# Optimization experiments

Hardware: AMD Instinct MI355X
Metric: run time of the kernel (lower is better)

## Reference

```python
import jax, jax.numpy as jnp
import numpy as np
from jax import lax

DIM, N_STATE, DT_RANK = 1024, 16, 64
BATCH, SEQ = 2, 2048


def setup_inputs() -> dict:
    key = jax.random.key(0)
    ks = jax.random.split(key, 12)
    s = 0.02
    x = jax.random.normal(ks[0], (BATCH, SEQ, DIM), dtype=jnp.float32)
    in_proj_w = jax.random.normal(ks[1], (2 * DIM, DIM), dtype=jnp.float32) * s
    conv_w = jax.random.normal(ks[2], (DIM, 1, 3), dtype=jnp.float32) * s
    conv_b = jax.random.normal(ks[3], (DIM,), dtype=jnp.float32) * s
    A_log = jax.random.normal(ks[4], (DIM, N_STATE), dtype=jnp.float32) * s
    D_param = jax.random.normal(ks[5], (DIM,), dtype=jnp.float32) * s
    x_proj_w = jax.random.normal(ks[6], (DT_RANK + 2 * N_STATE, DIM), dtype=jnp.float32) * s
    # dt_proj init mimics the torch module: bias = inv-softplus of dt in [dt_min, dt_max]
    dt = jnp.exp(jax.random.uniform(ks[7], (DIM,)) * (np.log(0.1) - np.log(0.001)) + np.log(0.001))
    dt = jnp.clip(dt, 0.0001, None)
    inv_dt = dt + jnp.log(-jnp.expm1(-dt))
    dt_init_std = DT_RANK ** (-0.5)
    dt_proj_w = jnp.tile(inv_dt[:, None], (1, DT_RANK)) * dt_init_std
    dt_proj_b = inv_dt
    out_proj_w = jax.random.normal(ks[8], (DIM, DIM), dtype=jnp.float32) * s
    return {
        "x": x, "in_proj_w": in_proj_w, "conv_w": conv_w, "conv_b": conv_b,
        "A_log": A_log, "D_param": D_param, "x_proj_w": x_proj_w,
        "dt_proj_w": dt_proj_w, "dt_proj_b": dt_proj_b, "out_proj_w": out_proj_w,
    }


def _selective_scan(u, delta, A, Bp, Cp, D_param):
    # u, delta: (B, L, D); A: (D, N); Bp, Cp: (B, L, N)
    deltaA = jnp.exp(delta[..., None] * A)                       # (B, L, D, N)
    deltaB_u = delta[..., None] * Bp[:, :, None, :] * u[..., None]  # (B, L, D, N)

    def step(state, inputs):
        dA_t, dBu_t, C_t = inputs          # (B, D, N), (B, D, N), (B, N)
        state = dA_t * state + dBu_t       # (B, D, N)
        y_t = jnp.einsum("bdn,bn->bd", state, C_t)
        return state, y_t

    init = jnp.zeros((u.shape[0], u.shape[2], A.shape[1]), dtype=u.dtype)
    xs = (jnp.swapaxes(deltaA, 0, 1), jnp.swapaxes(deltaB_u, 0, 1), jnp.swapaxes(Cp, 0, 1))
    _, ys = lax.scan(step, init, xs)       # ys: (L, B, D)
    y = jnp.swapaxes(ys, 0, 1)             # (B, L, D)
    return y + u * D_param


def reference(x, in_proj_w, conv_w, conv_b, A_log, D_param, x_proj_w, dt_proj_w, dt_proj_b, out_proj_w):
    B, L, D = x.shape
    xz = x @ in_proj_w.T                   # (B, L, 2D)
    xc, z = jnp.split(xz, 2, axis=-1)
    # depthwise conv1d, kernel 3, padding 1 (output length == L)
    xc = jnp.swapaxes(xc, 1, 2)            # (B, D, L)
    xc = lax.conv_general_dilated(
        xc, conv_w, window_strides=(1,), padding=[(1, 1)],
        dimension_numbers=("NCH", "OIH", "NCH"), feature_group_count=D,
    ) + conv_b[None, :, None]
    xc = jnp.swapaxes(xc, 1, 2)            # (B, L, D)
    x_dbl = xc @ x_proj_w.T                # (B, L, dt_rank + 2N)
    dt_r, Bp, Cp = jnp.split(x_dbl, [DT_RANK, DT_RANK + N_STATE], axis=-1)
    delta = jax.nn.softplus(dt_r @ dt_proj_w.T + dt_proj_b)   # (B, L, D)
    A = -jnp.exp(A_log)                    # (D, N)
    y = _selective_scan(xc, delta, A, Bp, Cp, D_param)
    y = y * jax.nn.silu(z)
    return y @ out_proj_w.T
```

## Files before the change

kernel.cpp:

```cpp
#include <hip/hip_runtime.h>
#include <math.h>

#define BATCH 2
#define SEQ   2048
#define DIM   1024
#define NST   16
#define DTR   64
#define KSL   8

typedef _Float16 f16x8 __attribute__((ext_vector_type(8)));
typedef float f32x4 __attribute__((ext_vector_type(4)));

__device__ __forceinline__ float softplus_f(float v) {
  return fmaxf(v, 0.f) + log1pf(expf(-fabsf(v)));
}
__device__ __forceinline__ float silu_f(float v) {
  return v / (1.f + expf(-v));
}

__device__ __forceinline__ void gl_lds16(const _Float16* g, _Float16* l) {
  __builtin_amdgcn_global_load_lds(
      (const __attribute__((address_space(1))) void*)g,
      (__attribute__((address_space(3))) void*)l, 16, 0, 0);
}

#define FMA_ROW(i, av)                                        \
  acc[i][0] = fmaf(av, b.x, acc[i][0]);                       \
  acc[i][1] = fmaf(av, b.y, acc[i][1]);                       \
  acc[i][2] = fmaf(av, b.z, acc[i][2]);                       \
  acc[i][3] = fmaf(av, b.w, acc[i][3]);

__global__ __launch_bounds__(256) void k_cvt(const float* __restrict__ in,
                                             _Float16* __restrict__ hi,
                                             _Float16* __restrict__ lo,
                                             int n) {
  const int i = (blockIdx.x * 256 + threadIdx.x) * 8;
  if (i >= n) return;
  const float4 a = *(const float4*)(in + i);
  const float4 b = *(const float4*)(in + i + 4);
  const float v[8] = {a.x, a.y, a.z, a.w, b.x, b.y, b.z, b.w};
  f16x8 h, l;
#pragma unroll
  for (int j = 0; j < 8; ++j) {
    const _Float16 hh = (_Float16)v[j];
    h[j] = hh;
    l[j] = (_Float16)(v[j] - (float)hh);
  }
  *(f16x8*)(hi + i) = h;
  *(f16x8*)(lo + i) = l;
}

template <int EPI>
__global__ __launch_bounds__(256) void kgemm_f16x3(
    const _Float16* __restrict__ Ah, const _Float16* __restrict__ Al,
    const _Float16* __restrict__ Bh, const _Float16* __restrict__ Bl,
    float* __restrict__ out0, float* __restrict__ out1) {
  __shared__ _Float16 sm[16384];
  _Float16* Ash = sm;
  _Float16* Asl = sm + 4096;
  _Float16* Bsh = sm + 8192;
  _Float16* Bsl = sm + 12288;

  const int tid = threadIdx.x;
  const int wid = tid >> 6, lane = tid & 63;
  const int wm = wid >> 1, wn = wid & 1;
  const int m0 = blockIdx.y * 128;
  const int n0 = blockIdx.x * 128;

  const int r0 = wid * 32;
  const int srow = lane >> 2;
  const int skq = (lane & 3) * 8;
  const _Float16* gAh = Ah + (size_t)(m0 + r0 + srow) * 1024 + skq;
  const _Float16* gAl = Al + (size_t)(m0 + r0 + srow) * 1024 + skq;
  const _Float16* gBh = Bh + (size_t)(n0 + r0 + srow) * 1024 + skq;
  const _Float16* gBl = Bl + (size_t)(n0 + r0 + srow) * 1024 + skq;
  _Float16* lAh = Ash + r0 * 32;
  _Float16* lAl = Asl + r0 * 32;
  _Float16* lBh = Bsh + r0 * 32;
  _Float16* lBl = Bsl + r0 * 32;

  const int fr = lane & 15;
  const int fk = (lane >> 4) * 8;

  f32x4 acc[4][4];
#pragma unroll
  for (int i = 0; i < 4; ++i)
#pragma unroll
    for (int j = 0; j < 4; ++j) acc[i][j] = (f32x4)(0.f);

  for (int k0 = 0; k0 < 1024; k0 += 32) {
    __syncthreads();
    gl_lds16(gAh + k0, lAh);
    gl_lds16(gAh + k0 + 16 * 1024, lAh + 512);
    gl_lds16(gAl + k0, lAl);
    gl_lds16(gAl + k0 + 16 * 1024, lAl + 512);
    gl_lds16(gBh + k0, lBh);
    gl_lds16(gBh + k0 + 16 * 1024, lBh + 512);
    gl_lds16(gBl + k0, lBl);
    gl_lds16(gBl + k0 + 16 * 1024, lBl + 512);
    __syncthreads();

    f16x8 ah[4], alo[4], bh[4], blo[4];
#pragma unroll
    for (int i = 0; i < 4; ++i) {
      const int ao = (wm * 64 + i * 16 + fr) * 32 + fk;
      const int bo = (wn * 64 + i * 16 + fr) * 32 + fk;
      ah[i]  = *(const f16x8*)(Ash + ao);
      alo[i] = *(const f16x8*)(Asl + ao);
      bh[i]  = *(const f16x8*)(Bsh + bo);
      blo[i] = *(const f16x8*)(Bsl + bo);
    }
#pragma unroll
    for (int i = 0; i < 4; ++i)
#pragma unroll
      for (int j = 0; j < 4; ++j) {
        acc[i][j] = __builtin_amdgcn_mfma_f32_16x16x32_f16(ah[i], bh[j],
                                                           acc[i][j], 0, 0, 0);
        acc[i][j] = __builtin_amdgcn_mfma_f32_16x16x32_f16(ah[i], blo[j],
                                                           acc[i][j], 0, 0, 0);
        acc[i][j] = __builtin_amdgcn_mfma_f32_16x16x32_f16(alo[i], bh[j],
                                                           acc[i][j], 0, 0, 0);
      }
  }

  const int lr4 = (lane >> 4) * 4, lc = lane & 15;
#pragma unroll
  for (int i = 0; i < 4; ++i) {
#pragma unroll
    for (int j = 0; j < 4; ++j) {
      const int ar = m0 + wm * 64 + i * 16 + lr4;
      const int bc = n0 + wn * 64 + j * 16 + lc;
#pragma unroll
      for (int r = 0; r < 4; ++r) {
        const float v = acc[i][j][r];
        if (EPI == 0) {
          out0[(size_t)(ar + r) * 1024 + bc] = v;
        } else {
          const int bb = bc >> 11, tt = bc & 2047;
          if (ar < 1024) {
            out0[((size_t)bb * 1024 + ar + r) * 2048 + tt] = v;
          } else {
            out1[((size_t)bb * 1024 + (ar + r - 1024)) * 2048 + tt] = v;
          }
        }
      }
    }
  }
}

__global__ __launch_bounds__(256) void k_conv(
    const float* __restrict__ xcraw, const float* __restrict__ cw,
    const float* __restrict__ cb, float* __restrict__ xc) {
  const int idx = blockIdx.x * 256 + threadIdx.x;
  const int t0 = (idx & (SEQ / 4 - 1)) * 4;
  const int r = idx >> 9;
  const int d = r & (DIM - 1);
  const float w0 = cw[d * 3 + 0], w1 = cw[d * 3 + 1], w2 = cw[d * 3 + 2];
  const float bias = cb[d];
  const float* in = xcraw + (size_t)r * SEQ;
  float o[4];
#pragma unroll
  for (int j = 0; j < 4; ++j) {
    const int t = t0 + j;
    const float xm = (t > 0) ? in[t - 1] : 0.f;
    const float x0 = in[t];
    const float xp = (t < SEQ - 1) ? in[t + 1] : 0.f;
    o[j] = fmaf(w0, xm, fmaf(w1, x0, fmaf(w2, xp, bias)));
  }
  *(float4*)(xc + (size_t)r * SEQ + t0) = make_float4(o[0], o[1], o[2], o[3]);
}

__global__ __launch_bounds__(256) void k2_xproj_sk(
    const float* __restrict__ xc, const float* __restrict__ wp,
    float* __restrict__ part) {
  __shared__ float As[16][100];
  __shared__ float Bs[16][132];
  const int tid = threadIdx.x;
  const int tile = blockIdx.x;
  const int ks = blockIdx.y;
  const int b = tile >> 4;
  const int t0 = (tile & 15) * 128;
  const int kbase = ks * (DIM / KSL);
  const int tx = tid & 15, ty = tid >> 4;
  float acc[6][8] = {{0.f}};
  for (int k = 0; k < DIM / KSL; k += 16) {
    float a_reg[6];
#pragma unroll
    for (int i = 0; i < 6; ++i) {
      const int ii = tid + 256 * i;
      a_reg[i] = wp[(size_t)(ii >> 4) * DIM + kbase + k + (ii & 15)];
    }
    float4 b_reg[2];
#pragma unroll
    for (int r = 0; r < 2; ++r) {
      const int id2 = tid + 256 * r;
      const int krow = id2 >> 5, t4 = (id2 & 31) * 4;
      b_reg[r] = *(const float4*)(xc + ((size_t)b * DIM + kbase + k + krow) *
                                           SEQ + t0 + t4);
    }
    __syncthreads();
#pragma unroll
    for (int i = 0; i < 6; ++i) {
      const int ii = tid + 256 * i;
      As[ii & 15][ii >> 4] = a_reg[i];
    }
#pragma unroll
    for (int r = 0; r < 2; ++r) {
      const int id2 = tid + 256 * r;
      const int krow = id2 >> 5, t4 = (id2 & 31) * 4;
      *(float4*)&Bs[krow][t4] = b_reg[r];
    }
    __syncthreads();
#pragma unroll
    for (int kk = 0; kk < 16; ++kk) {
      const float4 bA = *(const float4*)&Bs[kk][tx * 4];
      const float4 bB = *(const float4*)&Bs[kk][64 + tx * 4];
#pragma unroll
      for (int i = 0; i < 6; ++i) {
        const float a = As[kk][ty + 16 * i];
        acc[i][0] = fmaf(a, bA.x, acc[i][0]);
        acc[i][1] = fmaf(a, bA.y, acc[i][1]);
        acc[i][2] = fmaf(a, bA.z, acc[i][2]);
        acc[i][3] = fmaf(a, bA.w, acc[i][3]);
        acc[i][4] = fmaf(a, bB.x, acc[i][4]);
        acc[i][5] = fmaf(a, bB.y, acc[i][5]);
        acc[i][6] = fmaf(a, bB.z, acc[i][6]);
        acc[i][7] = fmaf(a, bB.w, acc[i][7]);
      }
    }
    __syncthreads();
  }
#pragma unroll
  for (int i = 0; i < 6; ++i) {
    const int j = ty + 16 * i;
    const size_t o = ((size_t)(ks * BATCH + b) * 96 + j) * SEQ + t0;
    *(float4*)(part + o + tx * 4) =
        make_float4(acc[i][0], acc[i][1], acc[i][2], acc[i][3]);
    *(float4*)(part + o + 64 + tx * 4) =
        make_float4(acc[i][4], acc[i][5], acc[i][6], acc[i][7]);
  }
}

__global__ __launch_bounds__(256) void k_red(const float* __restrict__ part,
                                             float* __restrict__ xdbl) {
  const size_t PL = (size_t)BATCH * 96 * SEQ;
  const size_t i4 = ((size_t)blockIdx.x * 256 + threadIdx.x) * 4;
  float4 s = *(const float4*)(part + i4);
#pragma unroll
  for (int ks = 1; ks < KSL; ++ks) {
    const float4 v = *(const float4*)(part + ks * PL + i4);
    s.x += v.x; s.y += v.y; s.z += v.z; s.w += v.w;
  }
  *(float4*)(xdbl + i4) = s;
}

__global__ __launch_bounds__(256) void k3_dtproj(
    const float* __restrict__ xdbl, const float* __restrict__ dtw,
    const float* __restrict__ dtb, float* __restrict__ delta) {
  __shared__ float As[16][68];
  __shared__ float Bs[16][68];
  const int tid = threadIdx.x;
  const int b = blockIdx.z;
  const int d0 = blockIdx.y * 64;
  const int t0 = blockIdx.x * 64;
  const int tx = tid & 15, ty = tid >> 4;
  const int lrow = tid >> 2, lcol = (tid & 3) * 4;
  const int bk = tid >> 4, bt4 = (tid & 15) * 4;
  float acc[4][4] = {{0.f}};
  for (int k = 0; k < DTR; k += 16) {
    const float4 av =
        *(const float4*)(dtw + (size_t)(d0 + lrow) * DTR + k + lcol);
    const float4 bv =
        *(const float4*)(xdbl + ((size_t)b * 96 + k + bk) * SEQ + t0 + bt4);
    __syncthreads();
    As[lcol + 0][lrow] = av.x; As[lcol + 1][lrow] = av.y;
    As[lcol + 2][lrow] = av.z; As[lcol + 3][lrow] = av.w;
    Bs[bk][bt4 + 0] = bv.x; Bs[bk][bt4 + 1] = bv.y;
    Bs[bk][bt4 + 2] = bv.z; Bs[bk][bt4 + 3] = bv.w;
    __syncthreads();
#pragma unroll
    for (int kk = 0; kk < 16; ++kk) {
      const float4 a = *(const float4*)&As[kk][ty * 4];
      const float4 b = *(const float4*)&Bs[kk][tx * 4];
      FMA_ROW(0, a.x) FMA_ROW(1, a.y) FMA_ROW(2, a.z) FMA_ROW(3, a.w)
    }
  }
#pragma unroll
  for (int i = 0; i < 4; ++i) {
    const int d = d0 + ty * 4 + i;
    const float bias = dtb[d];
    float4 v;
    v.x = softplus_f(acc[i][0] + bias);
    v.y = softplus_f(acc[i][1] + bias);
    v.z = softplus_f(acc[i][2] + bias);
    v.w = softplus_f(acc[i][3] + bias);
    *(float4*)(delta + ((size_t)b * DIM + d) * SEQ + t0 + tx * 4) = v;
  }
}

__global__ __launch_bounds__(1024) void k_scan_fused(
    const float* __restrict__ delta, const float* __restrict__ u,
    const float* __restrict__ xdbl, const float* __restrict__ A_log,
    const float* __restrict__ Dp, const float* __restrict__ z,
    float* __restrict__ y) {
  __shared__ float red[2][NST][512];
  const int tid = threadIdx.x;
  const int wv = tid >> 6;
  const int lane = tid & 63;
  const int idx = blockIdx.x;
  const int b = idx >> 10, d = idx & (DIM - 1);
  const float A = -expf(A_log[d * NST + wv]);
  const float Dprm = Dp[d];
  const float* drow = delta + (size_t)idx * SEQ;
  const float* urow = u + (size_t)idx * SEQ;
  const float* Brow = xdbl + ((size_t)b * 96 + DTR + wv) * SEQ;
  const float* Crow = xdbl + ((size_t)b * 96 + DTR + NST + wv) * SEQ;
  const float* zrow = z + (size_t)idx * SEQ;
  float* yrow = y + (size_t)idx * SEQ;
  float s_c = 0.f;
  const int tl = lane * 8;

  float4 dA = *(const float4*)(drow + tl);
  float4 dB = *(const float4*)(drow + tl + 4);
  float4 uA = *(const float4*)(urow + tl);
  float4 uB = *(const float4*)(urow + tl + 4);
  float4 bA = *(const float4*)(Brow + tl);
  float4 bB = *(const float4*)(Brow + tl + 4);

  for (int w = 0; w < SEQ / 512; ++w) {
    const int t0 = w * 512;
    const float4 cA = *(const float4*)(Crow + t0 + tl);
    const float4 cB = *(const float4*)(Crow + t0 + tl + 4);
    float p[8], q[8];
    {
      const float dls[8] = {dA.x, dA.y, dA.z, dA.w, dB.x, dB.y, dB.z, dB.w};
      const float us[8]  = {uA.x, uA.y, uA.z, uA.w, uB.x, uB.y, uB.z, uB.w};
      const float Bb[8]  = {bA.x, bA.y, bA.z, bA.w, bB.x, bB.y, bB.z, bB.w};
      p[0] = __expf(dls[0] * A);
      q[0] = dls[0] * us[0] * Bb[0];
#pragma unroll
      for (int i = 1; i < 8; ++i) {
        const float a = __expf(dls[i] * A);
        const float bq = dls[i] * us[i] * Bb[i];
        p[i] = a * p[i - 1];
        q[i] = fmaf(a, q[i - 1], bq);
      }
    }
    if (w + 1 < SEQ / 512) {
      const int tn = t0 + 512 + tl;
      dA = *(const float4*)(drow + tn);
      dB = *(const float4*)(drow + tn + 4);
      uA = *(const float4*)(urow + tn);
      uB = *(const float4*)(urow + tn + 4);
      bA = *(const float4*)(Brow + tn);
      bB = *(const float4*)(Brow + tn + 4);
    }
    float ia = p[7], ib = q[7];
#pragma unroll
    for (int sft = 1; sft < 64; sft <<= 1) {
      const float oa = __shfl_up(ia, sft, 64);
      const float ob = __shfl_up(ib, sft, 64);
      if (lane >= sft) { ib = fmaf(ia, ob, ib); ia = ia * oa; }
    }
    const float Wa = __shfl(ia, 63, 64);
    const float Wb = __shfl(ib, 63, 64);
    float ea = __shfl_up(ia, 1, 64);
    float eb = __shfl_up(ib, 1, 64);
    if (lane == 0) { ea = 1.f; eb = 0.f; }
    const float S = fmaf(ea, s_c, eb);
    s_c = fmaf(Wa, s_c, Wb);
    float4 y0, y1;
    y0.x = fmaf(p[0], S, q[0]) * cA.x;
    y0.y = fmaf(p[1], S, q[1]) * cA.y;
    y0.z = fmaf(p[2], S, q[2]) * cA.z;
    y0.w = fmaf(p[3], S, q[3]) * cA.w;
    y1.x = fmaf(p[4], S, q[4]) * cB.x;
    y1.y = fmaf(p[5], S, q[5]) * cB.y;
    y1.z = fmaf(p[6], S, q[6]) * cB.z;
    y1.w = fmaf(p[7], S, q[7]) * cB.w;
    *(float4*)&red[w & 1][wv][tl] = y0;
    *(float4*)&red[w & 1][wv][tl + 4] = y1;
    __syncthreads();
    if (tid < 512) {
      float sum = 0.f;
#pragma unroll
      for (int nn = 0; nn < NST; ++nn) sum += red[w & 1][nn][tid];
      const float uD = urow[t0 + tid];
      sum = fmaf(uD, Dprm, sum);
      const float zz = zrow[t0 + tid];
      const float sg = __builtin_amdgcn_rcpf(1.f + __expf(-zz));
      yrow[t0 + tid] = sum * zz * sg;
    }
  }
}

__global__ __launch_bounds__(256) void k_gt(
    const float* __restrict__ y, _Float16* __restrict__ gh,
    _Float16* __restrict__ gl) {
  __shared__ _Float16 th[64][68];
  __shared__ _Float16 tl[64][68];
  const int ti = threadIdx.x;
  const int t0 = blockIdx.x * 64;
  const int d0 = blockIdx.y * 64;
  const int b = blockIdx.z;
  const int c4 = (ti & 15) * 4;
#pragma unroll
  for (int rr = 0; rr < 4; ++rr) {
    const int dl_ = (ti >> 4) + 16 * rr;
    const size_t base = ((size_t)b * DIM + d0 + dl_) * SEQ + t0 + c4;
    const float4 yv = *(const float4*)(y + base);
    const float gy[4] = {yv.x, yv.y, yv.z, yv.w};
#pragma unroll
    for (int k = 0; k < 4; ++k) {
      const _Float16 h = (_Float16)gy[k];
      th[dl_][c4 + k] = h;
      tl[dl_][c4 + k] = (_Float16)(gy[k] - (float)h);
    }
  }
  __syncthreads();
#pragma unroll
  for (int rr = 0; rr < 2; ++rr) {
    const int chunk = ti + 256 * rr;
    const int tloc = chunk >> 3;
    const int dchunk = (chunk & 7) * 8;
    f16x8 hv, lv;
#pragma unroll
    for (int j = 0; j < 8; ++j) {
      hv[j] = th[dchunk + j][tloc];
      lv[j] = tl[dchunk + j][tloc];
    }
    const size_t o = ((size_t)b * SEQ + t0 + tloc) * DIM + d0 + dchunk;
    *(f16x8*)(gh + o) = hv;
    *(f16x8*)(gl + o) = lv;
  }
}

extern "C" void kernel_launch(void* const* d_in, const int* in_sizes, int n_in,
                              void* d_out, int out_size, void* d_ws,
                              size_t ws_size, hipStream_t stream) {
  const float* x          = (const float*)d_in[0];
  const float* in_proj_w  = (const float*)d_in[1];
  const float* conv_w     = (const float*)d_in[2];
  const float* conv_b     = (const float*)d_in[3];
  const float* A_log      = (const float*)d_in[4];
  const float* D_param    = (const float*)d_in[5];
  const float* x_proj_w   = (const float*)d_in[6];
  const float* dt_proj_w  = (const float*)d_in[7];
  const float* dt_proj_b  = (const float*)d_in[8];
  const float* out_proj_w = (const float*)d_in[9];
  float* out = (float*)d_out;
  float* ws = (float*)d_ws;

  const size_t PLANE = (size_t)BATCH * SEQ * DIM;
  float* xcraw = ws;
  float* delta = ws;
  _Float16* gh = (_Float16*)ws;
  _Float16* gl = (_Float16*)ws + PLANE;
  float* xc    = ws + PLANE;
  float* zbuf  = ws + 2 * PLANE;
  _Float16* xh = (_Float16*)(ws + 3 * PLANE);
  _Float16* xl = xh + PLANE;
  float* part  = ws + 3 * PLANE;
  float* ybuf  = ws + 3 * PLANE;
  float* xdbl  = ws + 4 * PLANE;
  _Float16* wih = (_Float16*)(ws + 4 * PLANE + 1572864);
  _Float16* wil = wih + (size_t)2 * DIM * DIM;
  _Float16* woh = wil + (size_t)2 * DIM * DIM;
  _Float16* wol = woh + (size_t)DIM * DIM;

  k_cvt<<<dim3(2048), 256, 0, stream>>>(x, xh, xl, BATCH * SEQ * DIM);
  k_cvt<<<dim3(1024), 256, 0, stream>>>(in_proj_w, wih, wil, 2 * DIM * DIM);
  k_cvt<<<dim3(512), 256, 0, stream>>>(out_proj_w, woh, wol, DIM * DIM);

  kgemm_f16x3<1><<<dim3(32, 16), 256, 0, stream>>>(wih, wil, xh, xl,
                                                   xcraw, zbuf);
  k_conv<<<dim3((BATCH * DIM * SEQ / 4) / 256), 256, 0, stream>>>(
      xcraw, conv_w, conv_b, xc);
  k2_xproj_sk<<<dim3(32, KSL), 256, 0, stream>>>(xc, x_proj_w, part);
  k_red<<<dim3(384), 256, 0, stream>>>(part, xdbl);
  k3_dtproj<<<dim3(SEQ / 64, DIM / 64, BATCH), 256, 0, stream>>>(
      xdbl, dt_proj_w, dt_proj_b, delta);
  k_scan_fused<<<dim3(BATCH * DIM), 1024, 0, stream>>>(
      delta, xc, xdbl, A_log, D_param, zbuf, ybuf);
  k_gt<<<dim3(SEQ / 64, DIM / 64, BATCH), 256, 0, stream>>>(ybuf, gh, gl);
  kgemm_f16x3<0><<<dim3(8, 32), 256, 0, stream>>>(gh, gl, woh, wol,
                                                  out, nullptr);
}
```

Baseline: 311.9 us.

## Double-buffer GEMM LDS staging with XOR swizzle, merge conversion kernels, pad scan reduction

The f16x3 GEMM now keeps two LDS stages, issuing the global-to-LDS loads for the next k-slice before computing on the current one. It also XOR-swizzles the k-chunk placement to reduce LDS bank conflicts on the fragment reads. The three fp32-to-f16 hi/lo conversion launches are merged into one kernel. The scan's cross-state reduction buffer is re-laid out with padding to cut bank conflicts. Risks: doubled LDS per block may lower occupancy, and the new code has no wait for the async LDS loads before they are read after the barrier.

After: 302.4 us. 1.03x faster.

```diff
diff --git a/kernel.cpp b/kernel.cpp
--- a/kernel.cpp
+++ b/kernel.cpp
@@ -14,9 +14,6 @@
 __device__ __forceinline__ float softplus_f(float v) {
   return fmaxf(v, 0.f) + log1pf(expf(-fabsf(v)));
 }
-__device__ __forceinline__ float silu_f(float v) {
-  return v / (1.f + expf(-v));
-}
 
 __device__ __forceinline__ void gl_lds16(const _Float16* g, _Float16* l) {
   __builtin_amdgcn_global_load_lds(
@@ -30,12 +27,24 @@
   acc[i][2] = fmaf(av, b.z, acc[i][2]);                       \
   acc[i][3] = fmaf(av, b.w, acc[i][3]);
 
-__global__ __launch_bounds__(256) void k_cvt(const float* __restrict__ in,
-                                             _Float16* __restrict__ hi,
-                                             _Float16* __restrict__ lo,
-                                             int n) {
-  const int i = (blockIdx.x * 256 + threadIdx.x) * 8;
-  if (i >= n) return;
+__global__ __launch_bounds__(256) void k_cvt3(
+    const float* __restrict__ in0, _Float16* __restrict__ hi0,
+    _Float16* __restrict__ lo0,
+    const float* __restrict__ in1, _Float16* __restrict__ hi1,
+    _Float16* __restrict__ lo1,
+    const float* __restrict__ in2, _Float16* __restrict__ hi2,
+    _Float16* __restrict__ lo2) {
+  int bb = blockIdx.x;
+  const float* in;
+  _Float16 *hi, *lo;
+  if (bb < 2048) {
+    in = in0; hi = hi0; lo = lo0;
+  } else if (bb < 3072) {
+    in = in1; hi = hi1; lo = lo1; bb -= 2048;
+  } else {
+    in = in2; hi = hi2; lo = lo2; bb -= 3072;
+  }
+  const int i = (bb * 256 + threadIdx.x) * 8;
   const float4 a = *(const float4*)(in + i);
   const float4 b = *(const float4*)(in + i + 4);
   const float v[8] = {a.x, a.y, a.z, a.w, b.x, b.y, b.z, b.w};
@@ -55,12 +64,7 @@
     const _Float16* __restrict__ Ah, const _Float16* __restrict__ Al,
     const _Float16* __restrict__ Bh, const _Float16* __restrict__ Bl,
     float* __restrict__ out0, float* __restrict__ out1) {
-  __shared__ _Float16 sm[16384];
-  _Float16* Ash = sm;
-  _Float16* Asl = sm + 4096;
-  _Float16* Bsh = sm + 8192;
-  _Float16* Bsl = sm + 12288;
-
+  __shared__ _Float16 sm[32768];
   const int tid = threadIdx.x;
   const int wid = tid >> 6, lane = tid & 63;
   const int wm = wid >> 1, wn = wid & 1;
@@ -69,18 +73,14 @@
 
   const int r0 = wid * 32;
   const int srow = lane >> 2;
-  const int skq = (lane & 3) * 8;
-  const _Float16* gAh = Ah + (size_t)(m0 + r0 + srow) * 1024 + skq;
-  const _Float16* gAl = Al + (size_t)(m0 + r0 + srow) * 1024 + skq;
-  const _Float16* gBh = Bh + (size_t)(n0 + r0 + srow) * 1024 + skq;
-  const _Float16* gBl = Bl + (size_t)(n0 + r0 + srow) * 1024 + skq;
-  _Float16* lAh = Ash + r0 * 32;
-  _Float16* lAl = Asl + r0 * 32;
-  _Float16* lBh = Bsh + r0 * 32;
-  _Float16* lBl = Bsl + r0 * 32;
+  const int skqs = ((lane & 3) ^ ((lane >> 3) & 3)) * 8;
+  const _Float16* gAh = Ah + (size_t)(m0 + r0 + srow) * 1024 + skqs;
+  const _Float16* gAl = Al + (size_t)(m0 + r0 + srow) * 1024 + skqs;
+  const _Float16* gBh = Bh + (size_t)(n0 + r0 + srow) * 1024 + skqs;
+  const _Float16* gBl = Bl + (size_t)(n0 + r0 + srow) * 1024 + skqs;
 
   const int fr = lane & 15;
-  const int fk = (lane >> 4) * 8;
+  const int fks = (((lane >> 4) ^ ((fr >> 1) & 3))) * 8;
 
   f32x4 acc[4][4];
 #pragma unroll
@@ -88,27 +88,35 @@
 #pragma unroll
     for (int j = 0; j < 4; ++j) acc[i][j] = (f32x4)(0.f);
 
+  auto STAGE = [&](int buf, int k0) {
+    _Float16* base = sm + buf * 16384;
+    _Float16* lA = base + r0 * 32;
+    gl_lds16(gAh + k0, lA);
+    gl_lds16(gAh + k0 + 16 * 1024, lA + 512);
+    gl_lds16(gAl + k0, lA + 4096);
+    gl_lds16(gAl + k0 + 16 * 1024, lA + 4096 + 512);
+    gl_lds16(gBh + k0, lA + 8192);
+    gl_lds16(gBh + k0 + 16 * 1024, lA + 8192 + 512);
+    gl_lds16(gBl + k0, lA + 12288);
+    gl_lds16(gBl + k0 + 16 * 1024, lA + 12288 + 512);
+  };
+
+  STAGE(0, 0);
+  int cur = 0;
   for (int k0 = 0; k0 < 1024; k0 += 32) {
     __syncthreads();
-    gl_lds16(gAh + k0, lAh);
-    gl_lds16(gAh + k0 + 16 * 1024, lAh + 512);
-    gl_lds16(gAl + k0, lAl);
-    gl_lds16(gAl + k0 + 16 * 1024, lAl + 512);
-    gl_lds16(gBh + k0, lBh);
-    gl_lds16(gBh + k0 + 16 * 1024, lBh + 512);
-    gl_lds16(gBl + k0, lBl);
-    gl_lds16(gBl + k0 + 16 * 1024, lBl + 512);
-    __syncthreads();
+    if (k0 + 32 < 1024) STAGE(cur ^ 1, k0 + 32);
+    const _Float16* base = sm + cur * 16384;
 
     f16x8 ah[4], alo[4], bh[4], blo[4];
 #pragma unroll
     for (int i = 0; i < 4; ++i) {
-      const int ao = (wm * 64 + i * 16 + fr) * 32 + fk;
-      const int bo = (wn * 64 + i * 16 + fr) * 32 + fk;
-      ah[i]  = *(const f16x8*)(Ash + ao);
-      alo[i] = *(const f16x8*)(Asl + ao);
-      bh[i]  = *(const f16x8*)(Bsh + bo);
-      blo[i] = *(const f16x8*)(Bsl + bo);
+      const int ao = (wm * 64 + i * 16 + fr) * 32 + fks;
+      const int bo = (wn * 64 + i * 16 + fr) * 32 + fks;
+      ah[i]  = *(const f16x8*)(base + ao);
+      alo[i] = *(const f16x8*)(base + 4096 + ao);
+      bh[i]  = *(const f16x8*)(base + 8192 + bo);
+      blo[i] = *(const f16x8*)(base + 12288 + bo);
     }
 #pragma unroll
     for (int i = 0; i < 4; ++i)
@@ -121,6 +129,7 @@
         acc[i][j] = __builtin_amdgcn_mfma_f32_16x16x32_f16(alo[i], bh[j],
                                                            acc[i][j], 0, 0, 0);
       }
+    cur ^= 1;
   }
 
   const int lr4 = (lane >> 4) * 4, lc = lane & 15;
@@ -303,7 +312,7 @@
     const float* __restrict__ xdbl, const float* __restrict__ A_log,
     const float* __restrict__ Dp, const float* __restrict__ z,
     float* __restrict__ y) {
-  __shared__ float red[2][NST][512];
+  __shared__ float red[2][NST][2][260];
   const int tid = threadIdx.x;
   const int wv = tid >> 6;
   const int lane = tid & 63;
@@ -319,6 +328,7 @@
   float* yrow = y + (size_t)idx * SEQ;
   float s_c = 0.f;
   const int tl = lane * 8;
+  const int tl2 = lane * 4;
 
   float4 dA = *(const float4*)(drow + tl);
   float4 dB = *(const float4*)(drow + tl + 4);
@@ -378,13 +388,15 @@
     y1.y = fmaf(p[5], S, q[5]) * cB.y;
     y1.z = fmaf(p[6], S, q[6]) * cB.z;
     y1.w = fmaf(p[7], S, q[7]) * cB.w;
-    *(float4*)&red[w & 1][wv][tl] = y0;
-    *(float4*)&red[w & 1][wv][tl + 4] = y1;
+    *(float4*)&red[w & 1][wv][0][tl2] = y0;
+    *(float4*)&red[w & 1][wv][1][tl2] = y1;
     __syncthreads();
     if (tid < 512) {
+      const int sub = (tid >> 2) & 1;
+      const int pos = ((tid >> 3) << 2) | (tid & 3);
       float sum = 0.f;
 #pragma unroll
-      for (int nn = 0; nn < NST; ++nn) sum += red[w & 1][nn][tid];
+      for (int nn = 0; nn < NST; ++nn) sum += red[w & 1][nn][sub][pos];
       const float uD = urow[t0 + tid];
       sum = fmaf(uD, Dprm, sum);
       const float zz = zrow[t0 + tid];
@@ -468,9 +480,8 @@
   _Float16* woh = wil + (size_t)2 * DIM * DIM;
   _Float16* wol = woh + (size_t)DIM * DIM;
 
-  k_cvt<<<dim3(2048), 256, 0, stream>>>(x, xh, xl, BATCH * SEQ * DIM);
-  k_cvt<<<dim3(1024), 256, 0, stream>>>(in_proj_w, wih, wil, 2 * DIM * DIM);
-  k_cvt<<<dim3(512), 256, 0, stream>>>(out_proj_w, woh, wol, DIM * DIM);
+  k_cvt3<<<dim3(3584), 256, 0, stream>>>(x, xh, xl, in_proj_w, wih, wil,
+                                         out_proj_w, woh, wol);
 
   kgemm_f16x3<1><<<dim3(32, 16), 256, 0, stream>>>(wih, wil, xh, xl,
                                                    xcraw, zbuf);
```
